# Kernel tuning notes

Measured on AMD Instinct MI355X. Metric: run time of the kernel, lower is better.

The kernel has to match this reference:

```python
import jax, jax.numpy as jnp
import numpy as np

B, S, D, H, DH = 2, 4096, 768, 12, 64
BS, NB, L, FF, VOCAB = 16, 256, 2, 3072, 50358
SCALE = 1.0 / np.sqrt(DH)


def _ln(x, g, b, eps=1e-12):
    m = jnp.mean(x, -1, keepdims=True)
    v = jnp.var(x, -1, keepdims=True)
    return (x - m) * jax.lax.rsqrt(v + eps) * g + b


def _make_key_block_idx(seed=0):
    rng = np.random.default_rng(seed)
    idx = np.zeros((NB, 7), np.int32)
    allb = np.arange(NB)
    for i in range(NB):
        req = sorted({0, NB - 1, max(i - 1, 0), i, min(i + 1, NB - 1)})
        pool = np.setdiff1d(allb, req)
        extra = rng.choice(pool, size=7 - len(req), replace=False)
        idx[i] = np.concatenate([req, extra])
    return jnp.asarray(idx)


def _sparse_attn(q, k, v, key_idx):
    # q,k,v: [B,H,NB,BS,DH]; key_idx: [NB,7]
    kg = k[:, :, key_idx].reshape(B, H, NB, 7 * BS, DH)  # gather key blocks
    vg = v[:, :, key_idx].reshape(B, H, NB, 7 * BS, DH)
    s = jnp.einsum('bhnqd,bhnkd->bhnqk', q, kg) * SCALE
    o = jnp.einsum('bhnqk,bhnkd->bhnqd', jax.nn.softmax(s, -1), vg)
    # first/last query blocks: full (global) attention over all keys
    qe = q[:, :, jnp.array([0, NB - 1])]                 # [B,H,2,BS,DH]
    kf = k.reshape(B, H, S, DH)
    vf = v.reshape(B, H, S, DH)
    se = jnp.einsum('bhgqd,bhkd->bhgqk', qe, kf) * SCALE
    oe = jnp.einsum('bhgqk,bhkd->bhgqd', jax.nn.softmax(se, -1), vf)
    o = o.at[:, :, 0].set(oe[:, :, 0]).at[:, :, NB - 1].set(oe[:, :, 1])
    # [B,H,NB,BS,DH] -> [B,S,D]
    return o.transpose(0, 2, 3, 1, 4).reshape(B, S, D)


def setup_inputs():
    key = jax.random.key(0)
    ks = iter(jax.random.split(key, 24))
    n = lambda sh, s=0.02: jax.random.normal(next(ks), sh, jnp.float32) * s
    inp = {
        'input_ids': jax.random.randint(next(ks), (B, S), 0, VOCAB),
        'key_block_idx': _make_key_block_idx(),
        'embed': n((VOCAB, D)),
        'Wqkv': n((L, D, 3 * D)), 'bqkv': jnp.zeros((L, 3 * D)),
        'Wo': n((L, D, D)), 'bo': jnp.zeros((L, D)),
        'ln1_g': jnp.ones((L, D)), 'ln1_b': jnp.zeros((L, D)),
        'Wff1': n((L, D, FF)), 'bff1': jnp.zeros((L, FF)),
        'Wff2': n((L, FF, D)), 'bff2': jnp.zeros((L, D)),
        'ln2_g': jnp.ones((L, D)), 'ln2_b': jnp.zeros((L, D)),
        'Wp': n((D, D)), 'bp': jnp.zeros((D,)),
        'start_w': jax.random.normal(next(ks), (D,)),
        'end_w': jax.random.normal(next(ks), (D,)),
        'd1_W': n((D, 20)), 'd1_b': jnp.zeros((20,)),
        'd2_W': n((20, 2)), 'd2_b': jnp.zeros((2,)),
    }
    return inp


def reference(input_ids, key_block_idx, embed, Wqkv, bqkv, Wo, bo, ln1_g, ln1_b,
              Wff1, bff1, Wff2, bff2, ln2_g, ln2_b, Wp, bp, start_w, end_w,
              d1_W, d1_b, d2_W, d2_b):
    x = embed[input_ids]                                  # [B,S,D]
    for l in range(L):
        qkv = x @ Wqkv[l] + bqkv[l]
        q, k, v = jnp.split(qkv, 3, axis=-1)
        blk = lambda t: t.reshape(B, NB, BS, H, DH).transpose(0, 3, 1, 2, 4)
        a = _sparse_attn(blk(q), blk(k), blk(v), key_block_idx)
        x = _ln(x + a @ Wo[l] + bo[l], ln1_g[l], ln1_b[l])
        h = jax.nn.gelu(x @ Wff1[l] + bff1[l]) @ Wff2[l] + bff2[l]
        x = _ln(x + h, ln2_g[l], ln2_b[l])
    pool = jnp.tanh(x[:, 0] @ Wp + bp)                    # BigBird pooler
    start_probs = jax.nn.softmax(x @ start_w, -1)         # [B,S]
    end_probs = jax.nn.softmax(x @ end_w, -1)
    d = (pool[0] @ d1_W + d1_b) @ d2_W + d2_b             # no ReLU, as in source
    disc = jax.nn.softmax(d, -1)
    return start_probs, end_probs, disc
```

## Files before the change

### kernel.cpp

```cpp
#include <hip/hip_runtime.h>
#include <hip/hip_bf16.h>
#include <math.h>

#define B_   2
#define S_   4096
#define D_   768
#define H_   12
#define DH_  64
#define BS_  16
#define NB_  256
#define FF_  3072
#define BT_  (B_ * S_)
#define SCALE_F 0.125f

#define NSPLIT 32
#define TILES_PER_SPLIT (NB_ / NSPLIT)
#define NEDGE (B_ * H_ * 2)
#define NSPARSE (B_ * H_ * NB_)
#define NXCD 8

typedef _Float16 f16x8 __attribute__((ext_vector_type(8)));
typedef _Float16 f16x4 __attribute__((ext_vector_type(4)));
typedef _Float16 f16x2 __attribute__((ext_vector_type(2)));
typedef float    f32x4 __attribute__((ext_vector_type(4)));
typedef float    f32x16 __attribute__((ext_vector_type(16)));

#define DKS 8
#define DKC (D_ / DKS)

#define MFMA_PV(a, b, c) __builtin_amdgcn_mfma_f32_16x16x16f16(a, b, c, 0, 0, 0)

__device__ __forceinline__ int xcd_swz(int bid, int nwg)
{
    int q = nwg / NXCD;
    return (bid % NXCD) * q + bid / NXCD;
}

#define GLD16(gp, lp) __builtin_amdgcn_global_load_lds( \
    (const __attribute__((address_space(1))) void*)(gp), \
    (__attribute__((address_space(3))) void*)(lp), 16, 0, 0)

__device__ __forceinline__ float fast_tanh(float z)
{
    float az = fabsf(z);
    float t = __expf(-2.0f * az);
    float r = (1.0f - t) / (1.0f + t);
    return z < 0.f ? -r : r;
}

__device__ __forceinline__ float gelu_tanh(float v)
{
    float v3 = v * v * v;
    return 0.5f * v * (1.0f + fast_tanh(0.79788456080286535588f * (v + 0.044715f * v3)));
}

struct WSeg { const float* src; _Float16* dst; int K; int N; int start; };
struct WSegs { WSeg s[8]; int total; };

__global__ __launch_bounds__(256) void prep_all(
    WSegs segs, const int* __restrict__ ids, const float* __restrict__ emb,
    _Float16* __restrict__ xh)
{
    int bt = blockIdx.x;
    int t = threadIdx.x;
    if (bt < segs.total) {
        __shared__ float tile[32][33];
        int si = 0;
#pragma unroll
        for (int u = 1; u < 8; ++u)
            if (bt >= segs.s[u].start) si = u;
        const WSeg& sg = segs.s[si];
        int tid = bt - sg.start;
        int tn = sg.N >> 5;
        int n0 = (tid % tn) * 32;
        int k0 = (tid / tn) * 32;

        {
            int r = t >> 3, c = (t & 7) * 4;
            f32x4 v = *(const f32x4*)&sg.src[(size_t)(k0 + r) * sg.N + n0 + c];
            tile[r][c + 0] = v[0];
            tile[r][c + 1] = v[1];
            tile[r][c + 2] = v[2];
            tile[r][c + 3] = v[3];
        }
        __syncthreads();
        {
            int r = t >> 3, c = (t & 7) * 4;
            f16x4 o;
            o[0] = (_Float16)tile[c + 0][r];
            o[1] = (_Float16)tile[c + 1][r];
            o[2] = (_Float16)tile[c + 2][r];
            o[3] = (_Float16)tile[c + 3][r];
            *(f16x4*)&sg.dst[(size_t)(n0 + r) * sg.K + k0 + c] = o;
        }
    } else {
        int row = bt - segs.total;
        int id = ids[row];
        const float* src = emb + (size_t)id * D_;
        _Float16* dst16 = xh + (size_t)row * D_;
        for (int d = t; d < D_; d += 256)
            dst16[d] = (_Float16)src[d];
    }
}

template<int MI, int DBUF, int ACT, int OUT16>
__global__ __launch_bounds__(256) void gemm_f16(
    const _Float16* __restrict__ A, const _Float16* __restrict__ Wt,
    const float* __restrict__ bias, void* __restrict__ Cp,
    int M, int N, int K, int NT128)
{
    constexpr int BM = MI * 64;
    constexpr int QA = 2 * MI;
    constexpr int ASZ = BM * 64;
    constexpr int BSZ = 128 * 64;

    __shared__ __attribute__((aligned(16))) _Float16 As[(DBUF ? 2 : 1) * ASZ];
    __shared__ __attribute__((aligned(16))) _Float16 Bs[(DBUF ? 2 : 1) * BSZ];

    int t = threadIdx.x;
    int w = t >> 6, l = t & 63;
    int swz = xcd_swz(blockIdx.x, gridDim.x);
    int bm = (swz / NT128) * BM, bn = (swz % NT128) * 128;
    int wr = (w >> 1) * (MI * 32), wc = (w & 1) * 64;

    f32x16 acc[MI][2];
#pragma unroll
    for (int i = 0; i < MI; ++i)
#pragma unroll
        for (int j = 0; j < 2; ++j)
#pragma unroll
            for (int r = 0; r < 16; ++r) acc[i][j][r] = 0.f;

    const _Float16* gA[QA];
    const _Float16* gB[4];
#pragma unroll
    for (int q = 0; q < QA; ++q) {
        int m = w * QA + q;
        int row = m * 8 + (l >> 3);
        int sc = (l & 7) ^ (row & 7);
        gA[q] = A + (size_t)(bm + row) * K + sc * 8;
    }
#pragma unroll
    for (int q = 0; q < 4; ++q) {
        int m = w * 4 + q;
        int row = m * 8 + (l >> 3);
        int sc = (l & 7) ^ (row & 7);
        gB[q] = Wt + (size_t)(bn + row) * K + sc * 8;
    }

    int aoff[4][MI], boff[4][2];
#pragma unroll
    for (int kk = 0; kk < 4; ++kk) {
        int ch = (kk * 2 + (l >> 5)) ^ (l & 7);
#pragma unroll
        for (int i = 0; i < MI; ++i)
            aoff[kk][i] = (wr + i * 32 + (l & 31)) * 64 + ch * 8;
#pragma unroll
        for (int j = 0; j < 2; ++j)
            boff[kk][j] = (wc + j * 32 + (l & 31)) * 64 + ch * 8;
    }

#define STAGE_(BUF, K0)                                                   \
    {                                                                     \
        _Float16* ab_ = As + (BUF) * ASZ;                                 \
        _Float16* bb_ = Bs + (BUF) * BSZ;                                 \
        _Pragma("unroll")                                                 \
        for (int q = 0; q < QA; ++q)                                      \
            GLD16(gA[q] + (K0), ab_ + (w * QA + q) * 512);                \
        _Pragma("unroll")                                                 \
        for (int q = 0; q < 4; ++q)                                       \
            GLD16(gB[q] + (K0), bb_ + (w * 4 + q) * 512);                 \
    }

#define COMPUTE_(BUF)                                                     \
    {                                                                     \
        const _Float16* ab_ = As + (BUF) * ASZ;                           \
        const _Float16* bb_ = Bs + (BUF) * BSZ;                           \
        _Pragma("unroll")                                                 \
        for (int kk = 0; kk < 4; ++kk) {                                  \
            f16x8 af[MI], bf[2];                                          \
            _Pragma("unroll")                                             \
            for (int i = 0; i < MI; ++i)                                  \
                af[i] = *(const f16x8*)(ab_ + aoff[kk][i]);               \
            _Pragma("unroll")                                             \
            for (int j = 0; j < 2; ++j)                                   \
                bf[j] = *(const f16x8*)(bb_ + boff[kk][j]);               \
            _Pragma("unroll")                                             \
            for (int i = 0; i < MI; ++i)                                  \
                _Pragma("unroll")                                         \
                for (int j = 0; j < 2; ++j)                               \
                    acc[i][j] = __builtin_amdgcn_mfma_f32_32x32x16_f16(   \
                        af[i], bf[j], acc[i][j], 0, 0, 0);                \
        }                                                                 \
    }

    if (DBUF) {
        STAGE_(0, 0);
        __syncthreads();
        int cur = 0;
#pragma unroll 2
        for (int k0 = 0; k0 < K; k0 += 64) {
            if (k0 + 64 < K) STAGE_(cur ^ 1, k0 + 64);
            COMPUTE_(cur);
            __syncthreads();
            cur ^= 1;
        }
    } else {
        for (int k0 = 0; k0 < K; k0 += 64) {
            STAGE_(0, k0);
            __syncthreads();
            COMPUTE_(0);
            __syncthreads();
        }
    }
#undef STAGE_
#undef COMPUTE_

#pragma unroll
    for (int i = 0; i < MI; ++i) {
#pragma unroll
        for (int j = 0; j < 2; ++j) {
            int col = bn + wc + j * 32 + (l & 31);
            float bv = bias[col];
#pragma unroll
            for (int rg = 0; rg < 4; ++rg) {
                int row0 = bm + wr + i * 32 + 8 * rg + 4 * (l >> 5);
#pragma unroll
                for (int r = 0; r < 4; ++r) {
                    float v = acc[i][j][rg * 4 + r] + bv;
                    if (ACT) v = gelu_tanh(v);
                    if (OUT16)
                        ((_Float16*)Cp)[(size_t)(row0 + r) * N + col] = (_Float16)v;
                    else
                        ((float*)Cp)[(size_t)(row0 + r) * N + col] = v;
                }
            }
        }
    }
}

template<int NT, bool EDGE>
__device__ __forceinline__ void attn_wave(
    const _Float16* __restrict__ qkv, const int* __restrict__ key_idx,
    _Float16* __restrict__ outp, float* __restrict__ pm,
    float* __restrict__ pl, float* __restrict__ pacc,
    int b, int h, int n, int split, int be,
    _Float16 (*vq)[24])
{
    int l = threadIdx.x & 63;
    int q = l & 15;
    int g = l >> 4;

    const _Float16* qp = qkv + ((size_t)(b * S_ + n * BS_ + q)) * (3 * D_) + h * DH_ + g * 8;
    f16x8 qf0 = *(const f16x8*)qp;
    f16x8 qf1 = *(const f16x8*)(qp + 32);

    float m_old = -1e30f, lsum = 0.f;
    f32x4 o[4];
#pragma unroll
    for (int db = 0; db < 4; ++db) o[db] = (f32x4){0.f, 0.f, 0.f, 0.f};

#pragma unroll 1
    for (int jj = 0; jj < NT; ++jj) {
        int kb = EDGE ? (split * NT + jj) : key_idx[n * 7 + jj];
        const _Float16* kvrow = qkv + ((size_t)(b * S_ + kb * BS_ + q)) * (3 * D_);

        f16x8 kf0 = *(const f16x8*)(kvrow + D_ + h * DH_ + g * 8);
        f16x8 kf1 = *(const f16x8*)(kvrow + D_ + h * DH_ + g * 8 + 32);

        {
            const _Float16* vp = kvrow + 2 * D_ + h * DH_ + g * 16;
            f16x8 v0 = *(const f16x8*)vp;
            f16x8 v1 = *(const f16x8*)(vp + 8);
#pragma unroll
            for (int u = 0; u < 8; ++u) vq[g * 16 + u][q] = v0[u];
#pragma unroll
            for (int u = 0; u < 8; ++u) vq[g * 16 + 8 + u][q] = v1[u];
        }

        f32x4 sc = (f32x4){0.f, 0.f, 0.f, 0.f};
        sc = __builtin_amdgcn_mfma_f32_16x16x32_f16(kf0, qf0, sc, 0, 0, 0);
        sc = __builtin_amdgcn_mfma_f32_16x16x32_f16(kf1, qf1, sc, 0, 0, 0);
#pragma unroll
        for (int r = 0; r < 4; ++r) sc[r] *= SCALE_F;

        float tm = fmaxf(fmaxf(sc[0], sc[1]), fmaxf(sc[2], sc[3]));
        tm = fmaxf(tm, __shfl_xor(tm, 16, 64));
        tm = fmaxf(tm, __shfl_xor(tm, 32, 64));
        float m_new = fmaxf(m_old, tm);

        float pr[4];
        float rs = 0.f;
#pragma unroll
        for (int r = 0; r < 4; ++r) { pr[r] = __expf(sc[r] - m_new); rs += pr[r]; }
        rs += __shfl_xor(rs, 16, 64);
        rs += __shfl_xor(rs, 32, 64);

        float corr = __expf(m_old - m_new);
        lsum = lsum * corr + rs;
        m_old = m_new;

        float cq[4];
#pragma unroll
        for (int r = 0; r < 4; ++r) cq[r] = __shfl(corr, g * 4 + r, 64);
#pragma unroll
        for (int db = 0; db < 4; ++db)
#pragma unroll
            for (int r = 0; r < 4; ++r) o[db][r] *= cq[r];

        f16x4 pa;
#pragma unroll
        for (int r = 0; r < 4; ++r) pa[r] = (_Float16)pr[r];

#pragma unroll
        for (int db = 0; db < 4; ++db) {
            f16x4 vb = *(const f16x4*)&vq[db * 16 + q][g * 4];
            o[db] = MFMA_PV(pa, vb, o[db]);
        }
    }

    if (EDGE) {
        int base16 = (be * NSPLIT + split) * 16;
        if (l < 16) { pm[base16 + l] = m_old; pl[base16 + l] = lsum; }
#pragma unroll
        for (int db = 0; db < 4; ++db)
#pragma unroll
            for (int r = 0; r < 4; ++r)
                pacc[(size_t)(base16 + g * 4 + r) * 64 + db * 16 + q] = o[db][r];
    } else {
        float linv[4];
#pragma unroll
        for (int r = 0; r < 4; ++r) linv[r] = 1.f / __shfl(lsum, g * 4 + r, 64);
#pragma unroll
        for (int r = 0; r < 4; ++r) {
            _Float16* dst = outp + ((size_t)(b * S_ + n * BS_ + g * 4 + r)) * D_ + h * DH_ + q;
#pragma unroll
            for (int db = 0; db < 4; ++db)
                dst[db * 16] = (_Float16)(o[db][r] * linv[r]);
        }
    }
}

__global__ __launch_bounds__(256) void attn_fused(
    const _Float16* __restrict__ qkv, const int* __restrict__ key_idx,
    _Float16* __restrict__ outp, float* __restrict__ pm,
    float* __restrict__ pl, float* __restrict__ pacc)
{
    __shared__ __attribute__((aligned(16))) _Float16 vqs[4][64][24];

    int w = threadIdx.x >> 6;
    int bi = xcd_swz(blockIdx.x, gridDim.x) * 4 + w;

    if (bi < NSPARSE) {
        int n = bi % NB_;
        if (n == 0 || n == NB_ - 1) return;
        int h = (bi / NB_) % H_;
        int b = bi / (NB_ * H_);
        attn_wave<7, false>(qkv, key_idx, outp, nullptr, nullptr, nullptr,
                            b, h, n, 0, 0, vqs[w]);
    } else {
        int ei = bi - NSPARSE;
        int split = ei % NSPLIT;
        int be = ei / NSPLIT;
        int e = be & 1;
        int h = (be >> 1) % H_;
        int b = be / (2 * H_);
        int n = e ? (NB_ - 1) : 0;
        attn_wave<TILES_PER_SPLIT, true>(qkv, nullptr, nullptr, pm, pl, pacc,
                                         b, h, n, split, be, vqs[w]);
    }
}

__global__ __launch_bounds__(256) void attn_edge_combine(
    const float* __restrict__ pm, const float* __restrict__ pl,
    const float* __restrict__ pacc, _Float16* __restrict__ outp)
{
    int be = blockIdx.x;
    int e = be & 1;
    int h = (be >> 1) % H_;
    int b = be / (2 * H_);
    int n = e ? (NB_ - 1) : 0;

    int t = threadIdx.x;
    int i = t >> 4;
    int c = t & 15;

    float M = -1e30f;
#pragma unroll 4
    for (int s = 0; s < NSPLIT; ++s)
        M = fmaxf(M, pm[(be * NSPLIT + s) * 16 + i]);

    float L = 0.f;
    float acc[4] = {0.f, 0.f, 0.f, 0.f};
    for (int s = 0; s < NSPLIT; ++s) {
        int ps = (be * NSPLIT + s) * 16 + i;
        float wgt = __expf(pm[ps] - M);
        L += pl[ps] * wgt;
#pragma unroll
        for (int u = 0; u < 4; ++u) acc[u] += pacc[(size_t)ps * 64 + c * 4 + u] * wgt;
    }

    float inv = 1.f / L;
    _Float16* dst = outp + ((size_t)(b * S_ + n * BS_ + i)) * D_ + h * DH_ + c * 4;
#pragma unroll
    for (int u = 0; u < 4; ++u) dst[u] = (_Float16)(acc[u] * inv);
}

template<int WRITE32>
__global__ __launch_bounds__(256) void add_ln_kernel(
    _Float16* __restrict__ xh, const _Float16* __restrict__ g,
    const float* __restrict__ gamma, const float* __restrict__ beta,
    float* __restrict__ x32)
{
    int row = blockIdx.x;
    int t = threadIdx.x;
    _Float16* xr = xh + (size_t)row * D_;
    const _Float16* gr = g + (size_t)row * D_;

    float v[3];
    float s = 0.f, s2 = 0.f;
#pragma unroll
    for (int r = 0; r < 3; ++r) {
        int d = t + 256 * r;
        v[r] = (float)xr[d] + (float)gr[d];
        s += v[r];
        s2 += v[r] * v[r];
    }
#pragma unroll
    for (int off = 32; off; off >>= 1) {
        s  += __shfl_xor(s, off, 64);
        s2 += __shfl_xor(s2, off, 64);
    }
    __shared__ float sA[4], sB[4];
    int wave = t >> 6, lane = t & 63;
    if (lane == 0) { sA[wave] = s; sB[wave] = s2; }
    __syncthreads();
    s  = sA[0] + sA[1] + sA[2] + sA[3];
    s2 = sB[0] + sB[1] + sB[2] + sB[3];
    float mean = s * (1.0f / D_);
    float var = s2 * (1.0f / D_) - mean * mean;
    float rstd = rsqrtf(var + 1e-12f);
#pragma unroll
    for (int r = 0; r < 3; ++r) {
        int d = t + 256 * r;
        float o = (v[r] - mean) * rstd * gamma[d] + beta[d];
        xr[d] = (_Float16)o;
        if (WRITE32) x32[(size_t)row * D_ + d] = o;
    }
}

__global__ __launch_bounds__(256) void heads_fused(
    const float* __restrict__ x, const float* __restrict__ sw,
    const float* __restrict__ ew, const float* __restrict__ Wp,
    float* __restrict__ sl, float* __restrict__ el,
    float* __restrict__ partial)
{
    int bi = blockIdx.x;
    int t = threadIdx.x;
    if (bi < 2048) {
        int wave = t >> 6, lane = t & 63;
        int row = bi * 4 + wave;
        const float* xr = x + (size_t)row * D_;
        float a = 0.f, e = 0.f;
        for (int d = lane; d < D_; d += 64) {
            float xv = xr[d];
            a += xv * sw[d];
            e += xv * ew[d];
        }
#pragma unroll
        for (int off = 32; off; off >>= 1) {
            a += __shfl_xor(a, off, 64);
            e += __shfl_xor(e, off, 64);
        }
        if (lane == 0) { sl[row] = a; el[row] = e; }
    } else {
        int ei = bi - 2048;
        int jb = ei % 3;
        int ks = ei / 3;
        int j = jb * 256 + t;
        int k0 = ks * DKC;

        __shared__ float xs[DKC];
        if (t < DKC) xs[t] = x[k0 + t];
        __syncthreads();

        float s = 0.f;
#pragma unroll 8
        for (int kk = 0; kk < DKC; ++kk)
            s += xs[kk] * Wp[(size_t)(k0 + kk) * D_ + j];
        partial[ks * D_ + j] = s;
    }
}

__global__ __launch_bounds__(256) void final_fused(
    const float* __restrict__ sl, const float* __restrict__ el,
    const float* __restrict__ partial, const float* __restrict__ bp,
    const float* __restrict__ d1W, const float* __restrict__ d1b,
    const float* __restrict__ d2W, const float* __restrict__ d2b,
    float* __restrict__ outp)
{
    int r = blockIdx.x;
    int t = threadIdx.x;
    if (r < 4) {
        const float* src = (r < 2 ? sl : el) + (size_t)(r & 1) * S_;
        float* dst = outp + (r < 2 ? 0 : BT_) + (size_t)(r & 1) * S_;
        int wave = t >> 6, lane = t & 63;
        __shared__ float sm[4], ss[4];

        float m = -1e30f;
        for (int k = t; k < S_; k += 256) m = fmaxf(m, src[k]);
#pragma unroll
        for (int off = 32; off; off >>= 1) m = fmaxf(m, __shfl_xor(m, off, 64));
        if (lane == 0) sm[wave] = m;
        __syncthreads();
        m = fmaxf(fmaxf(sm[0], sm[1]), fmaxf(sm[2], sm[3]));

        float s = 0.f;
        for (int k = t; k < S_; k += 256) s += __expf(src[k] - m);
#pragma unroll
        for (int off = 32; off; off >>= 1) s += __shfl_xor(s, off, 64);
        if (lane == 0) ss[wave] = s;
        __syncthreads();
        s = ss[0] + ss[1] + ss[2] + ss[3];

        float inv = 1.f / s;
        for (int k = t; k < S_; k += 256) dst[k] = __expf(src[k] - m) * inv;
    } else {
        __shared__ float pool[D_];
        __shared__ float h1[20];
        float* out2 = outp + 2 * BT_;
        for (int j = t; j < D_; j += 256) {
            float s = bp[j];
#pragma unroll
            for (int ks = 0; ks < DKS; ++ks) s += partial[ks * D_ + j];
            pool[j] = tanhf(s);
        }
        __syncthreads();
        if (t < 20) {
            float s = d1b[t];
            for (int k = 0; k < D_; ++k) s += pool[k] * d1W[k * 20 + t];
            h1[t] = s;
        }
        __syncthreads();
        if (t == 0) {
            float d0 = d2b[0], d1v = d2b[1];
#pragma unroll
            for (int u = 0; u < 20; ++u) {
                d0  += h1[u] * d2W[u * 2 + 0];
                d1v += h1[u] * d2W[u * 2 + 1];
            }
            float m = fmaxf(d0, d1v);
            float e0 = __expf(d0 - m), e1 = __expf(d1v - m);
            float inv = 1.f / (e0 + e1);
            out2[0] = e0 * inv;
            out2[1] = e1 * inv;
        }
    }
}

extern "C" void kernel_launch(void* const* d_in, const int* in_sizes, int n_in,
                              void* d_out, int out_size, void* d_ws, size_t ws_size,
                              hipStream_t stream)
{
    const int*   ids   = (const int*)d_in[0];
    const int*   kbi   = (const int*)d_in[1];
    const float* emb   = (const float*)d_in[2];
    const float* Wqkv  = (const float*)d_in[3];
    const float* bqkv  = (const float*)d_in[4];
    const float* Wo    = (const float*)d_in[5];
    const float* bo    = (const float*)d_in[6];
    const float* ln1g  = (const float*)d_in[7];
    const float* ln1b  = (const float*)d_in[8];
    const float* Wff1  = (const float*)d_in[9];
    const float* bff1  = (const float*)d_in[10];
    const float* Wff2  = (const float*)d_in[11];
    const float* bff2  = (const float*)d_in[12];
    const float* ln2g  = (const float*)d_in[13];
    const float* ln2b  = (const float*)d_in[14];
    const float* Wp    = (const float*)d_in[15];
    const float* bp    = (const float*)d_in[16];
    const float* sw    = (const float*)d_in[17];
    const float* ew    = (const float*)d_in[18];
    const float* d1W   = (const float*)d_in[19];
    const float* d1b   = (const float*)d_in[20];
    const float* d2W   = (const float*)d_in[21];
    const float* d2b   = (const float*)d_in[22];
    float* outp = (float*)d_out;

    float* ws   = (float*)d_ws;
    float* x    = ws;
    float* xbf  = x   + (size_t)BT_ * D_;
    float* r1f  = xbf + (size_t)BT_ * D_ / 2;
    float* abf  = r1f + (size_t)BT_ * FF_ / 2;
    float* r2   = abf + (size_t)BT_ * D_ / 2;
    float* wtf  = r2  + (size_t)BT_ * D_;
    float* sl   = wtf + 7077888;
    float* el   = sl  + BT_;
    float* dpar = el  + BT_;

    _Float16* xh    = (_Float16*)xbf;
    _Float16* qkv16 = (_Float16*)r1f;
    _Float16* h16   = (_Float16*)r1f;
    _Float16* ab    = (_Float16*)abf;
    float* pm   = r2;
    float* pl   = r2 + NEDGE * NSPLIT * 16;
    float* pacc = pl + NEDGE * NSPLIT * 16;
    _Float16* g16 = (_Float16*)r2;

    _Float16* Wt    = (_Float16*)wtf;
    _Float16* WqkvT = Wt;
    _Float16* WoT   = WqkvT + (size_t)2 * 2304 * 768;
    _Float16* Wff1T = WoT   + (size_t)2 * 768 * 768;
    _Float16* Wff2T = Wff1T + (size_t)2 * 3072 * 768;

    WSegs segs;
    int start = 0;
    for (int l = 0; l < 2; ++l) {
        int base = l * 4;
        segs.s[base + 0] = { Wqkv + (size_t)l * 768 * 2304,
                             WqkvT + (size_t)l * 2304 * 768, 768, 2304, start };
        start += (2304 / 32) * (768 / 32);
        segs.s[base + 1] = { Wo + (size_t)l * 768 * 768,
                             WoT + (size_t)l * 768 * 768, 768, 768, start };
        start += (768 / 32) * (768 / 32);
        segs.s[base + 2] = { Wff1 + (size_t)l * 768 * 3072,
                             Wff1T + (size_t)l * 3072 * 768, 768, 3072, start };
        start += (3072 / 32) * (768 / 32);
        segs.s[base + 3] = { Wff2 + (size_t)l * 3072 * 768,
                             Wff2T + (size_t)l * 768 * 3072, 3072, 768, start };
        start += (768 / 32) * (3072 / 32);
    }
    segs.total = start;

    prep_all<<<segs.total + BT_, 256, 0, stream>>>(segs, ids, emb, xh);

    for (int l = 0; l < 2; ++l) {
        gemm_f16<2,0,0,1><<<(BT_/128) * (2304/128), 256, 0, stream>>>(
            xh, WqkvT + (size_t)l * 2304 * 768, bqkv + (size_t)l * 3 * D_,
            qkv16, BT_, 3 * D_, D_, 2304/128);
        attn_fused<<<(NSPARSE + NEDGE * NSPLIT) / 4, 256, 0, stream>>>(
            qkv16, kbi, ab, pm, pl, pacc);
        attn_edge_combine<<<NEDGE, 256, 0, stream>>>(pm, pl, pacc, ab);
        gemm_f16<1,1,0,1><<<(BT_/64) * (768/128), 256, 0, stream>>>(
            ab, WoT + (size_t)l * 768 * 768, bo + (size_t)l * D_,
            g16, BT_, D_, D_, 768/128);
        add_ln_kernel<0><<<BT_, 256, 0, stream>>>(
            xh, g16, ln1g + (size_t)l * D_, ln1b + (size_t)l * D_, nullptr);
        gemm_f16<2,0,1,1><<<(BT_/128) * (3072/128), 256, 0, stream>>>(
            xh, Wff1T + (size_t)l * 3072 * 768, bff1 + (size_t)l * FF_,
            h16, BT_, FF_, D_, 3072/128);
        gemm_f16<1,1,0,1><<<(BT_/64) * (768/128), 256, 0, stream>>>(
            h16, Wff2T + (size_t)l * 768 * 3072, bff2 + (size_t)l * D_,
            g16, BT_, D_, FF_, 768/128);
        if (l == 1)
            add_ln_kernel<1><<<BT_, 256, 0, stream>>>(
                xh, g16, ln2g + (size_t)l * D_, ln2b + (size_t)l * D_, x);
        else
            add_ln_kernel<0><<<BT_, 256, 0, stream>>>(
                xh, g16, ln2g + (size_t)l * D_, ln2b + (size_t)l * D_, nullptr);
    }

    heads_fused<<<2048 + 3 * DKS, 256, 0, stream>>>(x, sw, ew, Wp, sl, el, dpar);
    final_fused<<<5, 256, 0, stream>>>(sl, el, dpar, bp, d1W, d1b, d2W, d2b, outp);
}
```

Before: 549.6 us.

## Write QKV GEMM output in head-major layout for contiguous attention loads

Measured after the change: 552.1 us. Within noise of the previous version (+0.5%).

```diff
diff --git a/kernel.cpp b/kernel.cpp
--- a/kernel.cpp
+++ b/kernel.cpp
@@ -19,6 +19,9 @@
 #define NSPARSE (B_ * H_ * NB_)
 #define NXCD 8
 
+#define QKVSTRIDE ((size_t)BT_ * 768)
+#define HSSZ ((size_t)S_ * 64)
+
 typedef _Float16 f16x8 __attribute__((ext_vector_type(8)));
 typedef _Float16 f16x4 __attribute__((ext_vector_type(4)));
 typedef _Float16 f16x2 __attribute__((ext_vector_type(2)));
@@ -103,7 +106,7 @@
     }
 }
 
-template<int MI, int DBUF, int ACT, int OUT16>
+template<int MI, int DBUF, int ACT, int OUTM>
 __global__ __launch_bounds__(256) void gemm_f16(
     const _Float16* __restrict__ A, const _Float16* __restrict__ Wt,
     const float* __restrict__ bias, void* __restrict__ Cp,
@@ -222,6 +225,13 @@
         for (int j = 0; j < 2; ++j) {
             int col = bn + wc + j * 32 + (l & 31);
             float bv = bias[col];
+            int which = 0, hh = 0, dd = 0;
+            if (OUTM == 2) {
+                which = (col >= 1536) ? 2 : ((col >= 768) ? 1 : 0);
+                int rem = col - which * 768;
+                hh = rem >> 6;
+                dd = rem & 63;
+            }
 #pragma unroll
             for (int rg = 0; rg < 4; ++rg) {
                 int row0 = bm + wr + i * 32 + 8 * rg + 4 * (l >> 5);
@@ -229,10 +239,16 @@
                 for (int r = 0; r < 4; ++r) {
                     float v = acc[i][j][rg * 4 + r] + bv;
                     if (ACT) v = gelu_tanh(v);
-                    if (OUT16)
+                    if (OUTM == 2) {
+                        int row = row0 + r;
+                        int bb = row >> 12, srow = row & 4095;
+                        ((_Float16*)Cp)[(size_t)(which * B_ * H_ + bb * H_ + hh) * HSSZ
+                                        + (size_t)srow * 64 + dd] = (_Float16)v;
+                    } else if (OUTM == 1) {
                         ((_Float16*)Cp)[(size_t)(row0 + r) * N + col] = (_Float16)v;
-                    else
+                    } else {
                         ((float*)Cp)[(size_t)(row0 + r) * N + col] = v;
+                    }
                 }
             }
         }
@@ -241,7 +257,7 @@
 
 template<int NT, bool EDGE>
 __device__ __forceinline__ void attn_wave(
-    const _Float16* __restrict__ qkv, const int* __restrict__ key_idx,
+    const _Float16* __restrict__ qkvp, const int* __restrict__ key_idx,
     _Float16* __restrict__ outp, float* __restrict__ pm,
     float* __restrict__ pl, float* __restrict__ pacc,
     int b, int h, int n, int split, int be,
@@ -251,7 +267,11 @@
     int q = l & 15;
     int g = l >> 4;
 
-    const _Float16* qp = qkv + ((size_t)(b * S_ + n * BS_ + q)) * (3 * D_) + h * DH_ + g * 8;
+    const _Float16* qh = qkvp + (size_t)(b * H_ + h) * HSSZ;
+    const _Float16* kh = qh + QKVSTRIDE;
+    const _Float16* vh = kh + QKVSTRIDE;
+
+    const _Float16* qp = qh + (size_t)(n * BS_ + q) * 64 + g * 8;
     f16x8 qf0 = *(const f16x8*)qp;
     f16x8 qf1 = *(const f16x8*)(qp + 32);
 
@@ -263,13 +283,13 @@
 #pragma unroll 1
     for (int jj = 0; jj < NT; ++jj) {
         int kb = EDGE ? (split * NT + jj) : key_idx[n * 7 + jj];
-        const _Float16* kvrow = qkv + ((size_t)(b * S_ + kb * BS_ + q)) * (3 * D_);
-
-        f16x8 kf0 = *(const f16x8*)(kvrow + D_ + h * DH_ + g * 8);
-        f16x8 kf1 = *(const f16x8*)(kvrow + D_ + h * DH_ + g * 8 + 32);
+        size_t tro = (size_t)(kb * BS_ + q) * 64;
+
+        f16x8 kf0 = *(const f16x8*)(kh + tro + g * 8);
+        f16x8 kf1 = *(const f16x8*)(kh + tro + g * 8 + 32);
 
         {
-            const _Float16* vp = kvrow + 2 * D_ + h * DH_ + g * 16;
+            const _Float16* vp = vh + tro + g * 16;
             f16x8 v0 = *(const f16x8*)vp;
             f16x8 v1 = *(const f16x8*)(vp + 8);
 #pragma unroll
@@ -342,7 +362,7 @@
 }
 
 __global__ __launch_bounds__(256) void attn_fused(
-    const _Float16* __restrict__ qkv, const int* __restrict__ key_idx,
+    const _Float16* __restrict__ qkvp, const int* __restrict__ key_idx,
     _Float16* __restrict__ outp, float* __restrict__ pm,
     float* __restrict__ pl, float* __restrict__ pacc)
 {
@@ -356,7 +376,7 @@
         if (n == 0 || n == NB_ - 1) return;
         int h = (bi / NB_) % H_;
         int b = bi / (NB_ * H_);
-        attn_wave<7, false>(qkv, key_idx, outp, nullptr, nullptr, nullptr,
+        attn_wave<7, false>(qkvp, key_idx, outp, nullptr, nullptr, nullptr,
                             b, h, n, 0, 0, vqs[w]);
     } else {
         int ei = bi - NSPARSE;
@@ -366,7 +386,7 @@
         int h = (be >> 1) % H_;
         int b = be / (2 * H_);
         int n = e ? (NB_ - 1) : 0;
-        attn_wave<TILES_PER_SPLIT, true>(qkv, nullptr, nullptr, pm, pl, pacc,
+        attn_wave<TILES_PER_SPLIT, true>(qkvp, nullptr, nullptr, pm, pl, pacc,
                                          b, h, n, split, be, vqs[w]);
     }
 }
@@ -635,7 +655,7 @@
     prep_all<<<segs.total + BT_, 256, 0, stream>>>(segs, ids, emb, xh);
 
     for (int l = 0; l < 2; ++l) {
-        gemm_f16<2,0,0,1><<<(BT_/128) * (2304/128), 256, 0, stream>>>(
+        gemm_f16<2,0,0,2><<<(BT_/128) * (2304/128), 256, 0, stream>>>(
             xh, WqkvT + (size_t)l * 2304 * 768, bqkv + (size_t)l * 3 * D_,
             qkv16, BT_, 3 * D_, D_, 2304/128);
         attn_fused<<<(NSPARSE + NEDGE * NSPLIT) / 4, 256, 0, stream>>>(
```
